# Kernel tuning notes

Hardware: AMD Instinct MI355X
Metric: run time of the kernel (lower is better)

Reference implementation:

```python
import jax, jax.numpy as jnp
import numpy as np

EMBED_DIM = 1024
NUM_HEADS = 8
HEAD_DIM = EMBED_DIM // NUM_HEADS
SEQ_LEN = 128              # T: leaf sequence length of the tree
NODE_LEN = 2 * SEQ_LEN - 1 # Tk: nodes of a binary tree over T leaves
BATCH = 4
TGT_LEN = 128


def _tree_spans(lo, hi, out):
    # spans (lo, hi) of a balanced binary constituency tree, lo <= hi
    out.append((lo, hi))
    if lo == hi:
        return
    mid = (lo + hi) // 2
    _tree_spans(lo, mid, out)
    _tree_spans(mid + 1, hi, out)


def setup_inputs() -> dict:
    key = jax.random.key(0)
    ks = jax.random.split(key, 6)
    query = jax.random.normal(ks[0], (TGT_LEN, BATCH, EMBED_DIM), jnp.float32)
    key_t = jax.random.normal(ks[1], (NODE_LEN, BATCH, EMBED_DIM), jnp.float32)
    value = jax.random.normal(ks[2], (NODE_LEN, BATCH, EMBED_DIM), jnp.float32)
    spans = []
    _tree_spans(0, SEQ_LEN - 1, spans)
    spans = np.asarray(spans, dtype=np.int64)            # [Tk, 2], row <= col
    indices = jnp.asarray(np.broadcast_to(spans[None], (BATCH, NODE_LEN, 2)).copy())
    s = 1.0 / np.sqrt(EMBED_DIM)  # xavier-ish scale
    in_proj_weight = jax.random.uniform(ks[3], (3 * EMBED_DIM, EMBED_DIM), jnp.float32, -s, s)
    in_proj_bias = jnp.zeros((3 * EMBED_DIM,), jnp.float32)
    out_proj_weight = jax.random.uniform(ks[4], (EMBED_DIM, EMBED_DIM), jnp.float32, -s, s)
    out_proj_bias = jnp.zeros((EMBED_DIM,), jnp.float32)
    return {"query": query, "key": key_t, "value": value, "indices": indices,
            "in_proj_weight": in_proj_weight, "in_proj_bias": in_proj_bias,
            "out_proj_weight": out_proj_weight, "out_proj_bias": out_proj_bias}


def _forward(query, key, value, indices, in_proj_weight, in_proj_bias,
             out_proj_weight, out_proj_bias):
    T, H, D = SEQ_LEN, NUM_HEADS, HEAD_DIM
    lq, B, E = query.shape
    Tk = key.shape[0]
    wq, wk, wv = jnp.split(in_proj_weight, 3, axis=0)
    bq, bk, bv = jnp.split(in_proj_bias, 3)
    q = (query @ wq.T + bq) * (D ** -0.5)   # scaling = head_dim ** -0.5
    k = key @ wk.T + bk
    v = value @ wv.T + bv

    def to_heads(x):  # [L, B, E] -> [B*H, L, D]
        L = x.shape[0]
        return x.reshape(L, B * H, D).transpose(1, 0, 2)

    q, k, v = to_heads(q), to_heads(k), to_heads(v)

    # indices2flat_indices: fl_idx = row * T + col  -> [B, Tk]
    fl_idx = indices[:, :, 0] * T + indices[:, :, 1]

    # seq2matrix: scatter node keys into [B, H, D, T*T] span matrix
    k_b = k.reshape(B, H, Tk, D)

    def scat(kb, fb):  # kb [H, Tk, D], fb [Tk]
        return jnp.zeros((H, D, T * T), kb.dtype).at[:, :, fb].set(kb.transpose(0, 2, 1))

    mat_k = jax.vmap(scat)(k_b, fl_idx).reshape(B * H, D, T, T)

    # query2matrix + dot product: affinity[b,q,r,c] = <q_bq, k_node(r,c)> * triu(r<=c)
    triu = jnp.triu(jnp.ones((T, T), q.dtype))
    aff = jnp.einsum('bqd,bdrc->bqrc', q, mat_k) * triu  # [B*H, lq, T, T]

    # DP (hierarchical) accumulation over contained spans:
    # acc[r,c] = sum_{r <= r' <= c' <= c} aff[r',c']
    acc = jnp.flip(jnp.cumsum(jnp.flip(aff, axis=2), axis=2), axis=2)
    acc = jnp.cumsum(acc, axis=3)

    # gather scores back at node span positions -> [B, H, lq, Tk]
    acc = acc.reshape(B, H, lq, T * T)
    scores = jnp.take_along_axis(acc, fl_idx[:, None, None, :], axis=3)

    w = jax.nn.softmax(scores.reshape(B * H, lq, Tk), axis=-1)
    attn = jnp.einsum('bqn,bnd->bqd', w, v)              # [B*H, lq, D]
    attn = attn.transpose(1, 0, 2).reshape(lq, B, E)
    return attn @ out_proj_weight.T + out_proj_bias


def reference(query, key, value, indices, in_proj_weight, in_proj_bias,
              out_proj_weight, out_proj_bias):
    return _forward(query, key, value, indices, in_proj_weight, in_proj_bias,
                    out_proj_weight, out_proj_bias)
```

## Files before the change

kernel.cpp:

```cpp
#include <hip/hip_runtime.h>
#include <math.h>

#define EMBED 1024
#define NHEAD 8
#define HDIM 128
#define TK 255
#define BATCH 4
#define LQ 128
#define BH 32

typedef __attribute__((ext_vector_type(4))) float f32x4;
typedef __attribute__((ext_vector_type(8))) short short8;
typedef __attribute__((ext_vector_type(4))) short short4v;

static __device__ __forceinline__ unsigned short f2bf(float f) {
    unsigned u = __float_as_uint(f);
    u += 0x7FFFu + ((u >> 16) & 1u);
    return (unsigned short)(u >> 16);
}
static __device__ __forceinline__ float bfbits2f(unsigned short s) {
    return __uint_as_float(((unsigned)s) << 16);
}

__global__ __launch_bounds__(256) void prep_kernel(
    const float* __restrict__ query, const float* __restrict__ key_t,
    const float* __restrict__ value, const float* __restrict__ ipw,
    const float* __restrict__ opw,
    unsigned short* __restrict__ apk, unsigned short* __restrict__ wpk)
{
    const int blk = blockIdx.x;
    const int t = threadIdx.x;
    if (blk < 128) {
        const int b = blk >> 5, eg = blk & 31;
        const int cl = t & 31, seg = t >> 5;
        const int e = eg * 32 + cl;
        __shared__ float tot[8][33];
        float vals[32];
        float acc = 0.f;
        const int nhi = seg * 32 + 31;
        #pragma unroll
        for (int i = 0; i < 32; ++i) {
            const int n = nhi - i;
            float v = 0.f;
            if (n < TK) v = key_t[(long)(n * 4 + b) * 1024 + e];
            acc += v;
            vals[i] = acc;
        }
        tot[seg][cl] = acc;
        __syncthreads();
        float add = 0.f;
        #pragma unroll
        for (int s = 0; s < 8; ++s) if (s > seg) add += tot[s][cl];
        #pragma unroll
        for (int i = 0; i < 32; ++i) {
            const int n = nhi - i;
            const float f = vals[i] + add;
            const unsigned short hv = f2bf(f);
            const unsigned short lv = f2bf(f - bfbits2f(hv));
            unsigned short* dst = apk + (long)(512 + b * 256 + n) * 2048 + e;
            dst[0] = hv;
            dst[1024] = lv;
        }
    } else {
        const int APKC = 1536 * 256;
        const int TOT = APKC + 4096 * 256;
        for (int idx = (blk - 128) * 256 + t; idx < TOT; idx += 2048 * 256) {
            const bool isA = idx < APKC;
            const int rel = isA ? idx : idx - APKC;
            const int row = rel >> 8, c4 = rel & 255;
            const float* src = nullptr; long srow = 0;
            unsigned short* dst;
            bool wlo = true;
            if (isA) {
                if (row < 512) { src = query; srow = row; dst = apk + (long)row * 2048; }
                else {
                    const int vr = row - 512;
                    dst = apk + (long)(1536 + vr) * 2048;
                    if (vr < 1020) { src = value; srow = vr; }
                }
            } else {
                dst = wpk + (long)row * 2048;
                if (row < 3072) { src = ipw; srow = row; }
                else { src = opw; srow = row - 3072; }
                wlo = (row < 2048);
            }
            float4 f = make_float4(0.f, 0.f, 0.f, 0.f);
            if (src) f = *(const float4*)(src + srow * 1024 + c4 * 4);
            const unsigned short h0 = f2bf(f.x), h1 = f2bf(f.y), h2 = f2bf(f.z), h3 = f2bf(f.w);
            short4v hv;
            hv[0] = (short)h0; hv[1] = (short)h1; hv[2] = (short)h2; hv[3] = (short)h3;
            *(short4v*)(dst + c4 * 4) = hv;
            if (wlo) {
                short4v lv;
                lv[0] = (short)f2bf(f.x - bfbits2f(h0));
                lv[1] = (short)f2bf(f.y - bfbits2f(h1));
                lv[2] = (short)f2bf(f.z - bfbits2f(h2));
                lv[3] = (short)f2bf(f.w - bfbits2f(h3));
                *(short4v*)(dst + 1024 + c4 * 4) = lv;
            }
        }
    }
}

template<int BM, int BN, int TERMS, int EPI>
__device__ __forceinline__ void bgemm2(
    const unsigned short* __restrict__ A,
    const unsigned short* __restrict__ B,
    const float* __restrict__ bias,
    void* __restrict__ Cv, long ldc, float scale,
    int m0, int n0, unsigned char* lds)
{
    constexpr int AH = 0;
    constexpr int AL = BM * 128;
    constexpr int BHo = 2 * BM * 128;
    constexpr int BLo = BHo + BN * 128;
    constexpr int FM2 = BM / 32, FN2 = BN / 32;
    constexpr int CA = BM / 32;
    constexpr int CB = BN / 32;
    const int t = threadIdx.x, lane = t & 63, wave = t >> 6;
    const int wm = wave >> 1, wn = wave & 1;

    f32x4 acc[FM2][FN2];
    #pragma unroll
    for (int i = 0; i < FM2; ++i)
        #pragma unroll
        for (int j = 0; j < FN2; ++j)
            #pragma unroll
            for (int e = 0; e < 4; ++e) acc[i][j][e] = 0.f;

    const int srow_a = t >> 3, su = t & 7;
    short8 rah[CA], ral[CA], rbh[CB], rbl[CB];

    #pragma unroll
    for (int c = 0; c < CA; ++c) {
        const long base = (long)(m0 + c * 32 + srow_a) * 2048 + su * 8;
        rah[c] = *(const short8*)(A + base);
        ral[c] = *(const short8*)(A + base + 1024);
    }
    #pragma unroll
    for (int c = 0; c < CB; ++c) {
        const long base = (long)(n0 + c * 32 + srow_a) * 2048 + su * 8;
        rbh[c] = *(const short8*)(B + base);
        if (TERMS == 3) rbl[c] = *(const short8*)(B + base + 1024);
    }

    for (int kt = 0; kt < 16; ++kt) {
        #pragma unroll
        for (int c = 0; c < CA; ++c) {
            const int row = c * 32 + srow_a;
            const int byte = row * 128 + ((su ^ (row & 7)) << 4);
            *(short8*)(lds + AH + byte) = rah[c];
            *(short8*)(lds + AL + byte) = ral[c];
        }
        #pragma unroll
        for (int c = 0; c < CB; ++c) {
            const int row = c * 32 + srow_a;
            const int byte = row * 128 + ((su ^ (row & 7)) << 4);
            *(short8*)(lds + BHo + byte) = rbh[c];
            if (TERMS == 3) *(short8*)(lds + BLo + byte) = rbl[c];
        }
        __syncthreads();
        if (kt + 1 < 16) {
            const int off = (kt + 1) * 64;
            #pragma unroll
            for (int c = 0; c < CA; ++c) {
                const long base = (long)(m0 + c * 32 + srow_a) * 2048 + off + su * 8;
                rah[c] = *(const short8*)(A + base);
                ral[c] = *(const short8*)(A + base + 1024);
            }
            #pragma unroll
            for (int c = 0; c < CB; ++c) {
                const long base = (long)(n0 + c * 32 + srow_a) * 2048 + off + su * 8;
                rbh[c] = *(const short8*)(B + base);
                if (TERMS == 3) rbl[c] = *(const short8*)(B + base + 1024);
            }
        }
        #pragma unroll
        for (int ks = 0; ks < 2; ++ks) {
            short8 afh[FM2], afl[FM2], bgh[FN2], bgl[FN2];
            #pragma unroll
            for (int fm = 0; fm < FM2; ++fm) {
                const int row = wm * (BM / 2) + fm * 16 + (lane & 15);
                const int byte = row * 128 + (((ks * 4 + (lane >> 4)) ^ (row & 7)) << 4);
                afh[fm] = *(const short8*)(lds + AH + byte);
                afl[fm] = *(const short8*)(lds + AL + byte);
            }
            #pragma unroll
            for (int fn = 0; fn < FN2; ++fn) {
                const int row = wn * (BN / 2) + fn * 16 + (lane & 15);
                const int byte = row * 128 + (((ks * 4 + (lane >> 4)) ^ (row & 7)) << 4);
                bgh[fn] = *(const short8*)(lds + BHo + byte);
                if (TERMS == 3) bgl[fn] = *(const short8*)(lds + BLo + byte);
            }
            #pragma unroll
            for (int fm = 0; fm < FM2; ++fm)
                #pragma unroll
                for (int fn = 0; fn < FN2; ++fn) {
                    acc[fm][fn] = __builtin_amdgcn_mfma_f32_16x16x32_bf16(afh[fm], bgh[fn], acc[fm][fn], 0, 0, 0);
                    acc[fm][fn] = __builtin_amdgcn_mfma_f32_16x16x32_bf16(afl[fm], bgh[fn], acc[fm][fn], 0, 0, 0);
                    if (TERMS == 3)
                        acc[fm][fn] = __builtin_amdgcn_mfma_f32_16x16x32_bf16(afh[fm], bgl[fn], acc[fm][fn], 0, 0, 0);
                }
        }
        __syncthreads();
    }

    #pragma unroll
    for (int fm = 0; fm < FM2; ++fm)
        #pragma unroll
        for (int i = 0; i < 4; ++i) {
            const int m = m0 + wm * (BM / 2) + fm * 16 + ((lane >> 4) << 2) + i;
            #pragma unroll
            for (int fn = 0; fn < FN2; ++fn) {
                const int n = n0 + wn * (BN / 2) + fn * 16 + (lane & 15);
                float v = acc[fm][fn][i];
                if (EPI == 0) {
                    float* C = (float*)Cv;
                    if (bias) v += bias[n];
                    C[(long)m * ldc + n] = v * scale;
                } else if (EPI == 1) {
                    float* C = (float*)Cv;
                    v += (float)(255 - (m & 255)) * bias[n];
                    C[(long)m * ldc + n] = v;
                } else if (EPI == 2) {
                    unsigned short* C = (unsigned short*)Cv;
                    const float val = (v + bias[n]) * scale;
                    const unsigned short hv = f2bf(val);
                    const unsigned short lv = f2bf(val - bfbits2f(hv));
                    C[(long)m * 2048 + n] = hv;
                    C[(long)m * 2048 + 1024 + n] = lv;
                } else {
                    unsigned short* C = (unsigned short*)Cv;
                    const float val = v + bias[n];
                    C[(long)m * 1024 + n] = f2bf(val);
                }
            }
        }
}

__global__ __launch_bounds__(256) void qkvb_kernel(
    const unsigned short* __restrict__ apk, const unsigned short* __restrict__ wpk,
    const float* __restrict__ ipb,
    unsigned short* __restrict__ qpk, float* __restrict__ sbuf,
    unsigned short* __restrict__ vpk, float qscale)
{
    __shared__ __align__(16) unsigned char lds[4 * 64 * 128];
    const int lid = blockIdx.y * 16 + blockIdx.x;
    const int xcd = lid & 7, slot = lid >> 3;
    const int y = xcd * 5 + (slot >> 4);
    const int x = slot & 15;
    if (y < 8) {
        bgemm2<64, 64, 3, 2>(apk, wpk, ipb, qpk, 2048, qscale,
                             y * 64, x * 64, lds);
    } else if (y < 24) {
        bgemm2<64, 64, 3, 1>(apk + 512L * 2048, wpk + 1024L * 2048, ipb + 1024, sbuf, 1024, 1.f,
                             (y - 8) * 64, x * 64, lds);
    } else {
        bgemm2<64, 64, 2, 3>(apk + 1536L * 2048, wpk + 2048L * 2048, ipb + 2048, vpk, 1024, 1.f,
                             (y - 24) * 64, x * 64, lds);
    }
}

__global__ __launch_bounds__(256) void outprojb_kernel(
    const unsigned short* __restrict__ apk2, const unsigned short* __restrict__ wpk,
    const float* __restrict__ opb, float* __restrict__ out)
{
    __shared__ __align__(16) unsigned char lds[(2 * 32 + 64) * 128];
    const int lid = blockIdx.x;
    const int xcd = lid & 7, slot = lid >> 3;
    const int y = xcd * 2 + (slot >> 4);
    const int x = slot & 15;
    bgemm2<32, 64, 2, 0>(apk2, wpk + 3072L * 2048, opb, out, 1024, 1.f,
                         y * 32, x * 64, lds);
}

#define F_QH 0
#define F_QL 4096
#define F_KH 8192
#define F_KL 24576
#define F_PH 40960
#define F_RED 49152
#define F_INV 49664

__global__ __launch_bounds__(256, 2) void fused_attn_kernel(
    const unsigned short* __restrict__ qpk, const float* __restrict__ sbuf,
    const unsigned short* __restrict__ vpk, const int* __restrict__ indices,
    unsigned short* __restrict__ apk2)
{
    __shared__ __align__(16) unsigned char lds[49728];
    __shared__ int onode[256];
    const int lid = blockIdx.x;
    const int xcd = lid & 7, slot = lid >> 3;
    const int bh = xcd * 4 + (slot >> 3), qq8 = slot & 7;
    const int b = bh >> 3, h = bh & 7;
    const int t = threadIdx.x, lane = t & 63, wn = t >> 6;
    float* red = (float*)(lds + F_RED);
    float* inv = (float*)(lds + F_INV);

    if (t < TK) {
        const int r0 = indices[(b * TK + t) * 2 + 0];
        const int c0 = indices[(b * TK + t) * 2 + 1];
        onode[t] = t + 2 * (c0 - r0) + 1;
    } else if (t < 256) {
        onode[t] = 255;
    }

    {
        #pragma unroll
        for (int rr = 0; rr < 2; ++rr) {
            const int chunk = rr * 256 + t;
            const int row = chunk >> 5;
            const int rem = chunk & 31;
            const int plane = rem >> 4, u = rem & 15;
            const int tq = qq8 * 16 + row;
            short8 v = *(const short8*)(qpk + (long)(tq * 4 + b) * 2048 + plane * 1024 + h * 128 + u * 8);
            const int byte = row * 256 + ((u ^ (row & 15)) << 4);
            *(short8*)(lds + (plane ? F_QL : F_QH) + byte) = v;
        }
    }

    f32x4 acc[4];
    #pragma unroll
    for (int nb = 0; nb < 4; ++nb)
        #pragma unroll
        for (int e = 0; e < 4; ++e) acc[nb][e] = 0.f;

    #pragma unroll
    for (int nb = 0; nb < 4; ++nb) {
        __syncthreads();
        {
            const int c4 = t & 31, r8 = t >> 5;
            const float* sb = sbuf + (long)b * 256 * 1024 + h * 128 + c4 * 4;
            #pragma unroll
            for (int rr = 0; rr < 8; ++rr) {
                const int nl = r8 + rr * 8;
                const int node = nb * 64 + nl;
                float4 f0 = *(const float4*)(sb + (long)node * 1024);
                float4 f1 = *(const float4*)(sb + (long)onode[node] * 1024);
                float4 f = make_float4(f0.x - f1.x, f0.y - f1.y, f0.z - f1.z, f0.w - f1.w);
                const unsigned short h0 = f2bf(f.x), h1 = f2bf(f.y), h2 = f2bf(f.z), h3 = f2bf(f.w);
                short4v hv, lv;
                hv[0] = (short)h0; hv[1] = (short)h1; hv[2] = (short)h2; hv[3] = (short)h3;
                lv[0] = (short)f2bf(f.x - bfbits2f(h0));
                lv[1] = (short)f2bf(f.y - bfbits2f(h1));
                lv[2] = (short)f2bf(f.z - bfbits2f(h2));
                lv[3] = (short)f2bf(f.w - bfbits2f(h3));
                const int byte = nl * 256 + ((((c4 >> 1) ^ (nl & 15)) << 4) | ((c4 & 1) << 3));
                *(short4v*)(lds + F_KH + byte) = hv;
                *(short4v*)(lds + F_KL + byte) = lv;
            }
        }
        __syncthreads();
        #pragma unroll
        for (int ks = 0; ks < 4; ++ks) {
            short8 ah, al, bh_, bl;
            {
                const int row = lane & 15;
                const int byte = row * 256 + (((ks * 4 + (lane >> 4)) ^ (row & 15)) << 4);
                ah = *(const short8*)(lds + F_QH + byte);
                al = *(const short8*)(lds + F_QL + byte);
            }
            {
                const int rown = wn * 16 + (lane & 15);
                const int byte = rown * 256 + (((ks * 4 + (lane >> 4)) ^ (rown & 15)) << 4);
                bh_ = *(const short8*)(lds + F_KH + byte);
                bl = *(const short8*)(lds + F_KL + byte);
            }
            acc[nb] = __builtin_amdgcn_mfma_f32_16x16x32_bf16(ah, bh_, acc[nb], 0, 0, 0);
            acc[nb] = __builtin_amdgcn_mfma_f32_16x16x32_bf16(al, bh_, acc[nb], 0, 0, 0);
            acc[nb] = __builtin_amdgcn_mfma_f32_16x16x32_bf16(ah, bl, acc[nb], 0, 0, 0);
        }
    }

    float pmax[4] = {-1e30f, -1e30f, -1e30f, -1e30f};
    #pragma unroll
    for (int nb = 0; nb < 4; ++nb)
        #pragma unroll
        for (int i = 0; i < 4; ++i) {
            const int col = nb * 64 + wn * 16 + (lane & 15);
            const float s = (col < TK) ? acc[nb][i] : -1e30f;
            pmax[i] = fmaxf(pmax[i], s);
        }
    #pragma unroll
    for (int off = 1; off < 16; off <<= 1)
        #pragma unroll
        for (int i = 0; i < 4; ++i) pmax[i] = fmaxf(pmax[i], __shfl_xor(pmax[i], off));
    if ((lane & 15) == 0) {
        #pragma unroll
        for (int i = 0; i < 4; ++i) {
            const int row = ((lane >> 4) << 2) + i;
            red[wn * 16 + row] = pmax[i];
        }
    }
    __syncthreads();
    float rm[4];
    #pragma unroll
    for (int i = 0; i < 4; ++i) {
        const int row = ((lane >> 4) << 2) + i;
        rm[i] = fmaxf(fmaxf(red[row], red[16 + row]), fmaxf(red[32 + row], red[48 + row]));
    }
    float psum[4] = {0.f, 0.f, 0.f, 0.f};
    #pragma unroll
    for (int nb = 0; nb < 4; ++nb)
        #pragma unroll
        for (int i = 0; i < 4; ++i) {
            const int col = nb * 64 + wn * 16 + (lane & 15);
            const int row = ((lane >> 4) << 2) + i;
            float p = 0.f;
            if (col < TK) p = __expf(acc[nb][i] - rm[i]);
            psum[i] += p;
            const unsigned short hp = f2bf(p);
            const int u = ((col >> 3) ^ ((row & 15) << 1));
            const int byte = row * 512 + (u << 4) + (col & 7) * 2;
            *(unsigned short*)(lds + F_PH + byte) = hp;
        }
    #pragma unroll
    for (int off = 1; off < 16; off <<= 1)
        #pragma unroll
        for (int i = 0; i < 4; ++i) psum[i] += __shfl_xor(psum[i], off);
    if ((lane & 15) == 0) {
        #pragma unroll
        for (int i = 0; i < 4; ++i) {
            const int row = ((lane >> 4) << 2) + i;
            red[64 + wn * 16 + row] = psum[i];
        }
    }
    __syncthreads();
    if (wn == 0 && (lane & 15) == 0) {
        #pragma unroll
        for (int i = 0; i < 4; ++i) {
            const int row = ((lane >> 4) << 2) + i;
            inv[row] = 1.f / (red[64 + row] + red[80 + row] + red[96 + row] + red[112 + row]);
        }
    }

    f32x4 accO[2];
    #pragma unroll
    for (int fn = 0; fn < 2; ++fn)
        #pragma unroll
        for (int e = 0; e < 4; ++e) accO[fn][e] = 0.f;

    #pragma unroll
    for (int nb = 0; nb < 4; ++nb) {
        __syncthreads();
        {
            const int c8 = t & 15, r16 = t >> 4;
            #pragma unroll
            for (int rr = 0; rr < 4; ++rr) {
                const int nl = r16 + rr * 16;
                const int node = nb * 64 + nl;
                short8 v = {0, 0, 0, 0, 0, 0, 0, 0};
                if (node < TK) v = *(const short8*)(vpk + (long)(node * 4 + b) * 1024 + h * 128 + c8 * 8);
                #pragma unroll
                for (int j = 0; j < 8; ++j) {
                    const int d = c8 * 8 + j;
                    const int byte = d * 128 + ((((nl >> 3) ^ (d & 7)) << 4) | ((nl & 7) << 1));
                    *(unsigned short*)(lds + F_KH + byte) = (unsigned short)v[j];
                }
            }
        }
        __syncthreads();
        #pragma unroll
        for (int ks = 0; ks < 2; ++ks) {
            short8 pa, vb[2];
            {
                const int row = lane & 15;
                const int u = (nb * 8 + ks * 4 + (lane >> 4)) ^ ((row & 15) << 1);
                const int byte = row * 512 + (u << 4);
                pa = *(const short8*)(lds + F_PH + byte);
            }
            #pragma unroll
            for (int fn = 0; fn < 2; ++fn) {
                const int d = wn * 32 + fn * 16 + (lane & 15);
                const int u = (ks * 4 + (lane >> 4)) ^ (d & 7);
                const int byte = d * 128 + (u << 4);
                vb[fn] = *(const short8*)(lds + F_KH + byte);
            }
            #pragma unroll
            for (int fn = 0; fn < 2; ++fn)
                accO[fn] = __builtin_amdgcn_mfma_f32_16x16x32_bf16(pa, vb[fn], accO[fn], 0, 0, 0);
        }
    }

    __syncthreads();
    #pragma unroll
    for (int i = 0; i < 4; ++i) {
        const int row = ((lane >> 4) << 2) + i;
        const float iv = inv[row];
        const int arow = (qq8 * 16 + row) * 4 + b;
        #pragma unroll
        for (int fn = 0; fn < 2; ++fn) {
            const int col = h * 128 + wn * 32 + fn * 16 + (lane & 15);
            const float val = accO[fn][i] * iv;
            const unsigned short hv = f2bf(val);
            const unsigned short lv = f2bf(val - bfbits2f(hv));
            apk2[(long)arow * 2048 + col] = hv;
            apk2[(long)arow * 2048 + 1024 + col] = lv;
        }
    }
}

extern "C" void kernel_launch(void* const* d_in, const int* in_sizes, int n_in,
                              void* d_out, int out_size, void* d_ws, size_t ws_size,
                              hipStream_t stream) {
    const float* query   = (const float*)d_in[0];
    const float* key_t   = (const float*)d_in[1];
    const float* value   = (const float*)d_in[2];
    const int*   indices = (const int*)d_in[3];
    const float* ipw     = (const float*)d_in[4];
    const float* ipb     = (const float*)d_in[5];
    const float* opw     = (const float*)d_in[6];
    const float* opb     = (const float*)d_in[7];
    float* out = (float*)d_out;

    float* ws = (float*)d_ws;
    float* sbuf = ws;
    unsigned short* qpk = (unsigned short*)(sbuf + 1048576);
    unsigned short* vpk = qpk + 512L * 2048;
    unsigned short* apk = vpk + 1024L * 1024;
    unsigned short* wpk = apk + 2560L * 2048;
    unsigned short* apk2 = apk;

    const float qscale = 0.08838834764831843f;

    prep_kernel<<<dim3(2176), 256, 0, stream>>>(query, key_t, value, ipw, opw, apk, wpk);

    qkvb_kernel<<<dim3(16, 40), 256, 0, stream>>>(apk, wpk, ipb, qpk, sbuf, vpk, qscale);

    fused_attn_kernel<<<dim3(256), 256, 0, stream>>>(qpk, sbuf, vpk, indices, apk2);

    outprojb_kernel<<<dim3(256), 256, 0, stream>>>(apk2, wpk, opb, out);
}
```

Baseline: 69.54 us.

## Stage GEMM tiles directly into double-buffered LDS via global_load_lds

Replaces register-staged global→LDS copies in the split-bf16 GEMM helper with async global_load_lds instructions, applying the XOR swizzle on the global source address so the LDS layout stays the same. LDS is double-buffered so the next k-tile loads while MFMAs consume the current one, and the first barrier per iteration is removed. This frees staging registers and overlaps memory with compute in the QKV and output projection kernels, at the cost of doubled LDS per block, which may reduce occupancy.

```diff
diff --git a/kernel.cpp b/kernel.cpp
--- a/kernel.cpp
+++ b/kernel.cpp
@@ -103,7 +103,7 @@
 }
 
 template<int BM, int BN, int TERMS, int EPI>
-__device__ __forceinline__ void bgemm2(
+__device__ __forceinline__ void bgemm3(
     const unsigned short* __restrict__ A,
     const unsigned short* __restrict__ B,
     const float* __restrict__ bias,
@@ -114,9 +114,11 @@
     constexpr int AL = BM * 128;
     constexpr int BHo = 2 * BM * 128;
     constexpr int BLo = BHo + BN * 128;
+    constexpr int BUFSZ = 2 * BM * 128 + 2 * BN * 128;
     constexpr int FM2 = BM / 32, FN2 = BN / 32;
-    constexpr int CA = BM / 32;
-    constexpr int CB = BN / 32;
+    constexpr int GA = BM / 8, GB = BN / 8;
+    constexpr int NI = 2 * GA + (TERMS == 3 ? 2 * GB : GB);
+    constexpr int IPW = NI / 4;
     const int t = threadIdx.x, lane = t & 63, wave = t >> 6;
     const int wm = wave >> 1, wn = wave & 1;
 
@@ -128,53 +130,32 @@
             #pragma unroll
             for (int e = 0; e < 4; ++e) acc[i][j][e] = 0.f;
 
-    const int srow_a = t >> 3, su = t & 7;
-    short8 rah[CA], ral[CA], rbh[CB], rbl[CB];
-
-    #pragma unroll
-    for (int c = 0; c < CA; ++c) {
-        const long base = (long)(m0 + c * 32 + srow_a) * 2048 + su * 8;
-        rah[c] = *(const short8*)(A + base);
-        ral[c] = *(const short8*)(A + base + 1024);
-    }
-    #pragma unroll
-    for (int c = 0; c < CB; ++c) {
-        const long base = (long)(n0 + c * 32 + srow_a) * 2048 + su * 8;
-        rbh[c] = *(const short8*)(B + base);
-        if (TERMS == 3) rbl[c] = *(const short8*)(B + base + 1024);
-    }
+    const int l8 = lane >> 3, lu = lane & 7;
+
+    auto stage = [&](int kt, int bufoff) {
+        #pragma unroll
+        for (int j = 0; j < IPW; ++j) {
+            const int q = wave * IPW + j;
+            const unsigned short* src; int srcoff, ldsoff, grp, rowbase;
+            if (q < GA)              { src = A; srcoff = 0;    ldsoff = AH;  grp = q;               rowbase = m0; }
+            else if (q < 2 * GA)     { src = A; srcoff = 1024; ldsoff = AL;  grp = q - GA;          rowbase = m0; }
+            else if (q < 2 * GA + GB){ src = B; srcoff = 0;    ldsoff = BHo; grp = q - 2 * GA;      rowbase = n0; }
+            else                     { src = B; srcoff = 1024; ldsoff = BLo; grp = q - 2 * GA - GB; rowbase = n0; }
+            const int rl = grp * 8 + l8;
+            const long gidx = (long)(rowbase + rl) * 2048 + srcoff + kt * 64 + ((lu ^ (rl & 7)) << 3);
+            __builtin_amdgcn_global_load_lds(
+                (const __attribute__((address_space(1))) void*)(src + gidx),
+                (__attribute__((address_space(3))) void*)(lds + bufoff + ldsoff + grp * 1024),
+                16, 0, 0);
+        }
+    };
+
+    stage(0, 0);
+    __syncthreads();
 
     for (int kt = 0; kt < 16; ++kt) {
-        #pragma unroll
-        for (int c = 0; c < CA; ++c) {
-            const int row = c * 32 + srow_a;
-            const int byte = row * 128 + ((su ^ (row & 7)) << 4);
-            *(short8*)(lds + AH + byte) = rah[c];
-            *(short8*)(lds + AL + byte) = ral[c];
-        }
-        #pragma unroll
-        for (int c = 0; c < CB; ++c) {
-            const int row = c * 32 + srow_a;
-            const int byte = row * 128 + ((su ^ (row & 7)) << 4);
-            *(short8*)(lds + BHo + byte) = rbh[c];
-            if (TERMS == 3) *(short8*)(lds + BLo + byte) = rbl[c];
-        }
-        __syncthreads();
-        if (kt + 1 < 16) {
-            const int off = (kt + 1) * 64;
-            #pragma unroll
-            for (int c = 0; c < CA; ++c) {
-                const long base = (long)(m0 + c * 32 + srow_a) * 2048 + off + su * 8;
-                rah[c] = *(const short8*)(A + base);
-                ral[c] = *(const short8*)(A + base + 1024);
-            }
-            #pragma unroll
-            for (int c = 0; c < CB; ++c) {
-                const long base = (long)(n0 + c * 32 + srow_a) * 2048 + off + su * 8;
-                rbh[c] = *(const short8*)(B + base);
-                if (TERMS == 3) rbl[c] = *(const short8*)(B + base + 1024);
-            }
-        }
+        const int cur = (kt & 1) * BUFSZ;
+        if (kt + 1 < 16) stage(kt + 1, ((kt + 1) & 1) * BUFSZ);
         #pragma unroll
         for (int ks = 0; ks < 2; ++ks) {
             short8 afh[FM2], afl[FM2], bgh[FN2], bgl[FN2];
@@ -182,15 +163,15 @@
             for (int fm = 0; fm < FM2; ++fm) {
                 const int row = wm * (BM / 2) + fm * 16 + (lane & 15);
                 const int byte = row * 128 + (((ks * 4 + (lane >> 4)) ^ (row & 7)) << 4);
-                afh[fm] = *(const short8*)(lds + AH + byte);
-                afl[fm] = *(const short8*)(lds + AL + byte);
+                afh[fm] = *(const short8*)(lds + cur + AH + byte);
+                afl[fm] = *(const short8*)(lds + cur + AL + byte);
             }
             #pragma unroll
             for (int fn = 0; fn < FN2; ++fn) {
                 const int row = wn * (BN / 2) + fn * 16 + (lane & 15);
                 const int byte = row * 128 + (((ks * 4 + (lane >> 4)) ^ (row & 7)) << 4);
-                bgh[fn] = *(const short8*)(lds + BHo + byte);
-                if (TERMS == 3) bgl[fn] = *(const short8*)(lds + BLo + byte);
+                bgh[fn] = *(const short8*)(lds + cur + BHo + byte);
+                if (TERMS == 3) bgl[fn] = *(const short8*)(lds + cur + BLo + byte);
             }
             #pragma unroll
             for (int fm = 0; fm < FM2; ++fm)
@@ -244,19 +225,19 @@
     unsigned short* __restrict__ qpk, float* __restrict__ sbuf,
     unsigned short* __restrict__ vpk, float qscale)
 {
-    __shared__ __align__(16) unsigned char lds[4 * 64 * 128];
+    __shared__ __align__(16) unsigned char lds[2 * (4 * 64 * 128)];
     const int lid = blockIdx.y * 16 + blockIdx.x;
     const int xcd = lid & 7, slot = lid >> 3;
     const int y = xcd * 5 + (slot >> 4);
     const int x = slot & 15;
     if (y < 8) {
-        bgemm2<64, 64, 3, 2>(apk, wpk, ipb, qpk, 2048, qscale,
+        bgemm3<64, 64, 3, 2>(apk, wpk, ipb, qpk, 2048, qscale,
                              y * 64, x * 64, lds);
     } else if (y < 24) {
-        bgemm2<64, 64, 3, 1>(apk + 512L * 2048, wpk + 1024L * 2048, ipb + 1024, sbuf, 1024, 1.f,
+        bgemm3<64, 64, 3, 1>(apk + 512L * 2048, wpk + 1024L * 2048, ipb + 1024, sbuf, 1024, 1.f,
                              (y - 8) * 64, x * 64, lds);
     } else {
-        bgemm2<64, 64, 2, 3>(apk + 1536L * 2048, wpk + 2048L * 2048, ipb + 2048, vpk, 1024, 1.f,
+        bgemm3<64, 64, 2, 3>(apk + 1536L * 2048, wpk + 2048L * 2048, ipb + 2048, vpk, 1024, 1.f,
                              (y - 24) * 64, x * 64, lds);
     }
 }
@@ -265,12 +246,12 @@
     const unsigned short* __restrict__ apk2, const unsigned short* __restrict__ wpk,
     const float* __restrict__ opb, float* __restrict__ out)
 {
-    __shared__ __align__(16) unsigned char lds[(2 * 32 + 64) * 128];
+    __shared__ __align__(16) unsigned char lds[2 * (2 * 32 * 128 + 2 * 64 * 128)];
     const int lid = blockIdx.x;
     const int xcd = lid & 7, slot = lid >> 3;
     const int y = xcd * 2 + (slot >> 4);
     const int x = slot & 15;
-    bgemm2<32, 64, 2, 0>(apk2, wpk + 3072L * 2048, opb, out, 1024, 1.f,
+    bgemm3<32, 64, 2, 0>(apk2, wpk + 3072L * 2048, opb, out, 1024, 1.f,
                          y * 32, x * 64, lds);
 }
 
```

Result: slower. 83.04 us (+19.4%).
